# Kernel tuning notes

Hardware: AMD Instinct MI355X
Metric: run time of the kernel (lower is better)

The kernel has to match this reference:

```python
import jax, jax.numpy as jnp
import numpy as np

D = 768          # model dim (ViT-Base)
H = 12           # num heads
DH = 64          # head dim
DFF = 4 * D      # mlp hidden
SMAX = 1024      # max sequence length in the packed batch
LENS = np.array([1024, 896, 768, 640, 512, 448, 256, 64], dtype=np.int32)
TOTAL = int(LENS.sum())  # 4608
LN_EPS = 1e-6
NEG = -1e30


def _ln(x, w, b):
    mu = jnp.mean(x, axis=-1, keepdims=True)
    var = jnp.mean(jnp.square(x - mu), axis=-1, keepdims=True)
    return (x - mu) * jax.lax.rsqrt(var + LN_EPS) * w + b


def setup_inputs() -> dict:
    key = jax.random.key(0)
    ks = jax.random.split(key, 16)
    s = 0.02
    cu = jnp.asarray(np.concatenate([[0], np.cumsum(LENS)]).astype(np.int32))
    return {
        "x": jax.random.normal(ks[0], (TOTAL, D), jnp.float32),
        "norm1_w": jnp.ones((D,), jnp.float32),
        "norm1_b": jnp.zeros((D,), jnp.float32),
        "qkv_w": jax.random.normal(ks[1], (3 * D, D), jnp.float32) * s,
        "qkv_b": jnp.zeros((3 * D,), jnp.float32),
        "proj_w": jax.random.normal(ks[2], (D, D), jnp.float32) * s,
        "proj_b": jnp.zeros((D,), jnp.float32),
        "ls1_gamma": jax.random.normal(ks[3], (D,), jnp.float32) * 0.1,
        "norm2_w": jnp.ones((D,), jnp.float32),
        "norm2_b": jnp.zeros((D,), jnp.float32),
        "fc1_w": jax.random.normal(ks[4], (DFF, D), jnp.float32) * s,
        "fc1_b": jnp.zeros((DFF,), jnp.float32),
        "fc2_w": jax.random.normal(ks[5], (D, DFF), jnp.float32) * s,
        "fc2_b": jnp.zeros((D,), jnp.float32),
        "ls2_gamma": jax.random.normal(ks[6], (D,), jnp.float32) * 0.1,
        "cu_seqlens": cu,
    }


def reference(x, norm1_w, norm1_b, qkv_w, qkv_b, proj_w, proj_b, ls1_gamma,
              norm2_w, norm2_b, fc1_w, fc1_b, fc2_w, fc2_b, ls2_gamma,
              cu_seqlens):
    total = x.shape[0]
    B = cu_seqlens.shape[0] - 1
    tok = jnp.arange(total)
    seg = jnp.searchsorted(cu_seqlens[1:], tok, side="right")  # [Total]
    pos = tok - cu_seqlens[seg]                                 # [Total]
    lens = cu_seqlens[1:] - cu_seqlens[:-1]                     # [B]

    # --- attention branch ---
    xn = _ln(x, norm1_w, norm1_b)
    qkv = (xn @ qkv_w.T + qkv_b).reshape(total, 3, H, DH)
    q, k, v = qkv[:, 0], qkv[:, 1], qkv[:, 2]                   # [Total,H,DH]

    # pad packed ragged tokens to [B, SMAX, H, DH]
    def pad(t):
        return jnp.zeros((B, SMAX, H, DH), t.dtype).at[seg, pos].set(t)
    qp, kp, vp = pad(q), pad(k), pad(v)

    valid = jnp.arange(SMAX)[None, :] < lens[:, None]           # [B,SMAX]
    scores = jnp.einsum("bqhd,bkhd->bhqk", qp, kp) * (DH ** -0.5)
    scores = jnp.where(valid[:, None, None, :], scores, NEG)
    attn = jax.nn.softmax(scores, axis=-1)
    out = jnp.einsum("bhqk,bkhd->bqhd", attn, vp)
    out = out[seg, pos].reshape(total, D)                       # back to packed

    attn_out = out @ proj_w.T + proj_b
    x = x + ls1_gamma * attn_out

    # --- mlp branch ---
    xn2 = _ln(x, norm2_w, norm2_b)
    h = jax.nn.gelu(xn2 @ fc1_w.T + fc1_b, approximate=False)
    h = h @ fc2_w.T + fc2_b
    return x + ls2_gamma * h
```

## Files before the change

### kernel.cpp

```cpp
#include <hip/hip_runtime.h>
#include <hip/hip_bf16.h>
#include <stdint.h>

#define D 768
#define HEADS 12
#define DHEAD 64
#define DFF 3072
#define TOTAL 4608
#define NSEG 8

typedef __bf16 bf16;
typedef __bf16 bf16x8 __attribute__((ext_vector_type(8)));
typedef __bf16 bf16x4 __attribute__((ext_vector_type(4)));
typedef float f32x4 __attribute__((ext_vector_type(4)));

__device__ __forceinline__ void gld_lds16(const void* g, void* l) {
  __builtin_amdgcn_global_load_lds(
      (const __attribute__((address_space(1))) void*)g,
      (__attribute__((address_space(3))) void*)(uintptr_t)l, 16, 0, 0);
}

__global__ __launch_bounds__(256) void cvt_all_kernel(
    const float* __restrict__ a, const float* __restrict__ b,
    const float* __restrict__ c, const float* __restrict__ d,
    bf16* __restrict__ out, int nA, int nAB, int nABC, int nTot) {
  int i = blockIdx.x * blockDim.x + threadIdx.x;
  if (i >= nTot) return;
  const float* src;
  int j;
  if (i < nA) { src = a; j = i; }
  else if (i < nAB) { src = b; j = i - nA; }
  else if (i < nABC) { src = c; j = i - nAB; }
  else { src = d; j = i - nABC; }
  float4 v = ((const float4*)src)[j];
  bf16x4 o;
  o[0] = (bf16)v.x; o[1] = (bf16)v.y; o[2] = (bf16)v.z; o[3] = (bf16)v.w;
  ((bf16x4*)out)[i] = o;
}

__global__ __launch_bounds__(256) void ln_kernel(
    const float* __restrict__ x, const float* __restrict__ w,
    const float* __restrict__ b, bf16* __restrict__ out) {
  __shared__ float red[8];
  int row = blockIdx.x;
  const float* xr = x + (size_t)row * D;
  int t = threadIdx.x;
  float v[3];
  float s = 0.f, s2 = 0.f;
#pragma unroll
  for (int j = 0; j < 3; j++) {
    v[j] = xr[t + 256 * j];
    s += v[j]; s2 += v[j] * v[j];
  }
#pragma unroll
  for (int m = 1; m <= 32; m <<= 1) {
    s += __shfl_xor(s, m);
    s2 += __shfl_xor(s2, m);
  }
  int wave = t >> 6, lane = t & 63;
  if (lane == 0) { red[wave] = s; red[4 + wave] = s2; }
  __syncthreads();
  s = red[0] + red[1] + red[2] + red[3];
  s2 = red[4] + red[5] + red[6] + red[7];
  float mu = s * (1.f / 768.f);
  float var = s2 * (1.f / 768.f) - mu * mu;
  float rstd = rsqrtf(var + 1e-6f);
#pragma unroll
  for (int j = 0; j < 3; j++) {
    int c = t + 256 * j;
    out[(size_t)row * D + c] = (bf16)((v[j] - mu) * rstd * w[c] + b[c]);
  }
}

__device__ __forceinline__ float fast_gelu(float v) {
  float u = v * (0.7978845608f + 0.0356774081f * v * v);
  float e = exp2f(2.8853900818f * u);
  float th = 1.f - 2.f * __builtin_amdgcn_rcpf(1.f + e);
  return 0.5f * v * (1.f + th);
}

template <int MODE, int TN, int BK, int GX, int GY>
__global__ __launch_bounds__(512, 4) void gemm_kernel(
    const bf16* __restrict__ A, const bf16* __restrict__ W,
    const float* __restrict__ bias, const float* __restrict__ res,
    const float* __restrict__ gamma, bf16* __restrict__ outb,
    float* __restrict__ outf, int N, int K) {
  constexpr int WNW = (TN == 128) ? 4 : 2;
  constexpr int WMW = 8 / WNW;
  constexpr int MI = 128 / 16 / WMW;
  constexpr int NJ = TN / 16 / WNW;
  constexpr int KH = BK / 32;
  constexpr int CG = BK / 8;
  constexpr int SH = 0;
  constexpr int LPR = BK / 8;
  constexpr int RS = 64 / LPR;
  constexpr int RA = 128 / 8;
  constexpr int RB = TN / 8;
  __shared__ __align__(16) bf16 As[2][128 * BK];
  __shared__ __align__(16) bf16 Bs[2][TN * BK];

  const int g = blockIdx.x;
  const int xc = g & 7, q = g >> 3;
  const int bx = q % GX, by = xc + 8 * (q / GX);
  if (by >= GY) return;
  const int m0 = by * 128, n0 = bx * TN;

  const int t = threadIdx.x, wave = t >> 6, lane = t & 63;
  const int quad = lane >> 4, l16 = lane & 15;
  const int wm = (wave % WMW) * (MI * 16), wn = (wave / WMW) * (NJ * 16);

  const int ar = lane / LPR, ac = lane % LPR;
  const int acg = ac ^ (((wave * RA + ar) >> SH) & (CG - 1));
  const int bcg = ac ^ (((wave * RB + ar) >> SH) & (CG - 1));
  const bf16* gA = A + (size_t)(m0 + wave * RA + ar) * K + acg * 8;
  const bf16* gB = W + (size_t)(n0 + wave * RB + ar) * K + bcg * 8;

  auto stage = [&](int buf) {
#pragma unroll
    for (int n = 0; n < RA / RS; n++)
      gld_lds16(gA + (size_t)n * RS * K, &As[buf][(wave * RA + n * RS) * BK]);
#pragma unroll
    for (int n = 0; n < RB / RS; n++)
      gld_lds16(gB + (size_t)n * RS * K, &Bs[buf][(wave * RB + n * RS) * BK]);
    gA += BK; gB += BK;
  };

  stage(0);

  f32x4 acc[MI][NJ] = {};
  int cur = 0;
  for (int k0 = 0; k0 < K; k0 += BK) {
    __syncthreads();
    if (k0 + BK < K) stage(cur ^ 1);
    const bf16* as = As[cur];
    const bf16* bs = Bs[cur];
    bf16x8 af[KH][MI], bg[KH][NJ];
#pragma unroll
    for (int kh = 0; kh < KH; kh++) {
#pragma unroll
      for (int i = 0; i < MI; i++) {
        int R = wm + i * 16 + l16;
        af[kh][i] = *(const bf16x8*)&as[R * BK + 8 * ((kh * 4 + quad) ^ ((R >> SH) & (CG - 1)))];
      }
#pragma unroll
      for (int j = 0; j < NJ; j++) {
        int R = wn + j * 16 + l16;
        bg[kh][j] = *(const bf16x8*)&bs[R * BK + 8 * ((kh * 4 + quad) ^ ((R >> SH) & (CG - 1)))];
      }
    }
#pragma unroll
    for (int kh = 0; kh < KH; kh++)
#pragma unroll
      for (int i = 0; i < MI; i++)
#pragma unroll
        for (int j = 0; j < NJ; j++)
          acc[i][j] = __builtin_amdgcn_mfma_f32_16x16x32_bf16(af[kh][i], bg[kh][j], acc[i][j], 0, 0, 0);
    cur ^= 1;
  }

#pragma unroll
  for (int i = 0; i < MI; i++)
#pragma unroll
    for (int j = 0; j < NJ; j++)
#pragma unroll
      for (int r = 0; r < 4; r++) {
        int row = m0 + wm + i * 16 + quad * 4 + r;
        int col = n0 + wn + j * 16 + l16;
        float v = acc[i][j][r] + bias[col];
        if (MODE == 0) {
          outb[(size_t)row * N + col] = (bf16)v;
        } else if (MODE == 1) {
          outf[(size_t)row * N + col] = res[(size_t)row * N + col] + gamma[col] * v;
        } else {
          outb[(size_t)row * N + col] = (bf16)fast_gelu(v);
        }
      }
}

#define KCH 8
#define QT2 52

__global__ __launch_bounds__(256) void attn_kernel(
    const bf16* __restrict__ qkv, const int* __restrict__ cu,
    bf16* __restrict__ attn, float* __restrict__ Opart,
    float* __restrict__ lpart) {
  __shared__ __align__(16) bf16 Ks[64][72];
  __shared__ __align__(16) bf16 VTs[64][64];

  const int qt = blockIdx.x, h = blockIdx.y, ch = blockIdx.z;
  const int tok0 = qt * 64;
  int b = 0;
  while (cu[b + 1] <= tok0) b++;
  const int s0 = cu[b], S = cu[b + 1] - s0;

  const int ntile = S >> 6;
  const int nchunk = (ntile + KCH - 1) / KCH;
  if (ch >= nchunk) return;
  const int t0 = ch * KCH;
  const int t1 = (t0 + KCH < ntile) ? t0 + KCH : ntile;

  const int t = threadIdx.x, wave = t >> 6, lane = t & 63;
  const int quad = lane >> 4, l16 = lane & 15;

  const size_t qrow = (size_t)(tok0 + wave * 16 + l16) * (3 * D) + h * 64;
  const bf16x8 bq0 = *(const bf16x8*)&qkv[qrow + quad * 8];
  const bf16x8 bq1 = *(const bf16x8*)&qkv[qrow + 32 + quad * 8];

  const int srow = t >> 2, sc0 = (t & 3) * 16;
  const size_t kbase = (size_t)(s0 + srow) * (3 * D) + h * 64 + sc0 + D;
  const int vr0 = (t & 15) * 4, vd0 = (t >> 4) * 4;
  const size_t vbase = (size_t)(s0 + vr0) * (3 * D) + h * 64 + vd0 + 2 * D;
  const int kB0 = ((vr0 >> 5) << 5) | (((vr0 >> 2) & 3) << 3) | (((vr0 >> 4) & 1) << 2);

  bf16x8 kr0 = *(const bf16x8*)&qkv[kbase + (size_t)t0 * 64 * (3 * D)];
  bf16x8 kr1 = *(const bf16x8*)&qkv[kbase + (size_t)t0 * 64 * (3 * D) + 8];
  bf16x4 vp[4];
#pragma unroll
  for (int i = 0; i < 4; i++)
    vp[i] = *(const bf16x4*)&qkv[vbase + (size_t)t0 * 64 * (3 * D) + (size_t)i * (3 * D)];

  f32x4 Oacc[4] = {};
  float li = 0.f;
  const float SC = 0.125f * 1.44269504089f;
  const int vsw = (l16 & 7) * 8;

  for (int it = t0; it < t1; it++) {
    __syncthreads();
    *(bf16x8*)&Ks[srow][sc0] = kr0;
    *(bf16x8*)&Ks[srow][sc0 + 8] = kr1;
#pragma unroll
    for (int j = 0; j < 4; j++) {
      int d = vd0 + j;
      bf16x4 w;
      w[0] = vp[0][j]; w[1] = vp[1][j]; w[2] = vp[2][j]; w[3] = vp[3][j];
      *(bf16x4*)&VTs[d][kB0 ^ ((d & 7) * 8)] = w;
    }
    __syncthreads();

    if (it + 1 < t1) {
      const size_t koff = kbase + (size_t)(it + 1) * 64 * (3 * D);
      const size_t voff = vbase + (size_t)(it + 1) * 64 * (3 * D);
      kr0 = *(const bf16x8*)&qkv[koff];
      kr1 = *(const bf16x8*)&qkv[koff + 8];
#pragma unroll
      for (int i = 0; i < 4; i++)
        vp[i] = *(const bf16x4*)&qkv[voff + (size_t)i * (3 * D)];
    }

    f32x4 sac[4];
#pragma unroll
    for (int nt = 0; nt < 4; nt++) {
      bf16x8 ak0 = *(const bf16x8*)&Ks[nt * 16 + l16][quad * 8];
      bf16x8 ak1 = *(const bf16x8*)&Ks[nt * 16 + l16][32 + quad * 8];
      f32x4 z = {};
      z = __builtin_amdgcn_mfma_f32_16x16x32_bf16(ak0, bq0, z, 0, 0, 0);
      sac[nt] = __builtin_amdgcn_mfma_f32_16x16x32_bf16(ak1, bq1, z, 0, 0, 0);
    }

    bf16x8 bv0, bv1;
    float ls = 0.f;
#pragma unroll
    for (int r = 0; r < 4; r++) {
      float e0 = exp2f(sac[0][r] * SC);
      float e1 = exp2f(sac[1][r] * SC);
      float e2 = exp2f(sac[2][r] * SC);
      float e3 = exp2f(sac[3][r] * SC);
      ls += (e0 + e1) + (e2 + e3);
      bv0[r] = (bf16)e0; bv0[4 + r] = (bf16)e1;
      bv1[r] = (bf16)e2; bv1[4 + r] = (bf16)e3;
    }
    li += ls;

#pragma unroll
    for (int dt = 0; dt < 4; dt++) {
      bf16x8 av0 = *(const bf16x8*)&VTs[dt * 16 + l16][(quad * 8) ^ vsw];
      bf16x8 av1 = *(const bf16x8*)&VTs[dt * 16 + l16][(32 + quad * 8) ^ vsw];
      Oacc[dt] = __builtin_amdgcn_mfma_f32_16x16x32_bf16(av0, bv0, Oacc[dt], 0, 0, 0);
      Oacc[dt] = __builtin_amdgcn_mfma_f32_16x16x32_bf16(av1, bv1, Oacc[dt], 0, 0, 0);
    }
  }

  li += __shfl_xor(li, 16);
  li += __shfl_xor(li, 32);
  const int q = wave * 16 + l16;

  if (nchunk == 1) {
    const float inv = 1.f / li;
#pragma unroll
    for (int dt = 0; dt < 4; dt++) {
      bf16x4 w;
#pragma unroll
      for (int r = 0; r < 4; r++) w[r] = (bf16)(Oacc[dt][r] * inv);
      *(bf16x4*)&attn[(size_t)(tok0 + q) * D + h * 64 + dt * 16 + quad * 4] = w;
    }
  } else {
    const int slot = (h * QT2 + qt) * 2 + ch;
    float* op = Opart + (size_t)slot * 4096;
#pragma unroll
    for (int dt = 0; dt < 4; dt++)
      *(f32x4*)&op[q * 64 + dt * 16 + quad * 4] = Oacc[dt];
    if (quad == 0) lpart[(size_t)slot * 64 + q] = li;
  }
}

__global__ __launch_bounds__(256) void attn_reduce_kernel(
    const float* __restrict__ Opart, const float* __restrict__ lpart,
    const int* __restrict__ cu, bf16* __restrict__ attn) {
  const int qt = blockIdx.x, h = blockIdx.y;
  const int tok0 = qt * 64;
  int b = 0;
  while (cu[b + 1] <= tok0) b++;
  const int ntile = (cu[b + 1] - cu[b]) >> 6;
  if (ntile <= KCH) return;

  const int t = threadIdx.x, q = t >> 2, c0 = (t & 3) * 16;
  const int slot0 = (h * QT2 + qt) * 2;
  const float li = lpart[(size_t)slot0 * 64 + q] + lpart[(size_t)(slot0 + 1) * 64 + q];
  const float inv = 1.f / li;
  const float* p0 = Opart + (size_t)slot0 * 4096 + q * 64 + c0;
  const float* p1 = p0 + 4096;
  bf16x8 o0, o1;
#pragma unroll
  for (int g = 0; g < 4; g++) {
    f32x4 a = *(const f32x4*)&p0[g * 4];
    f32x4 c = *(const f32x4*)&p1[g * 4];
#pragma unroll
    for (int r = 0; r < 4; r++) {
      bf16 v = (bf16)((a[r] + c[r]) * inv);
      if (g < 2) o0[g * 4 + r] = v; else o1[(g - 2) * 4 + r] = v;
    }
  }
  const size_t ob = (size_t)(tok0 + q) * D + h * 64 + c0;
  *(bf16x8*)&attn[ob] = o0;
  *(bf16x8*)&attn[ob + 8] = o1;
}

extern "C" void kernel_launch(void* const* d_in, const int* in_sizes, int n_in,
                              void* d_out, int out_size, void* d_ws,
                              size_t ws_size, hipStream_t stream) {
  const float* x       = (const float*)d_in[0];
  const float* norm1_w = (const float*)d_in[1];
  const float* norm1_b = (const float*)d_in[2];
  const float* qkv_w   = (const float*)d_in[3];
  const float* qkv_b   = (const float*)d_in[4];
  const float* proj_w  = (const float*)d_in[5];
  const float* proj_b  = (const float*)d_in[6];
  const float* ls1     = (const float*)d_in[7];
  const float* norm2_w = (const float*)d_in[8];
  const float* norm2_b = (const float*)d_in[9];
  const float* fc1_w   = (const float*)d_in[10];
  const float* fc1_b   = (const float*)d_in[11];
  const float* fc2_w   = (const float*)d_in[12];
  const float* fc2_b   = (const float*)d_in[13];
  const float* ls2     = (const float*)d_in[14];
  const int*   cu      = (const int*)d_in[15];
  float* out = (float*)d_out;

  char* ws = (char*)d_ws;
  size_t off = 0;
  auto alloc = [&](size_t bytes) {
    void* p = ws + off;
    off += (bytes + 255) & ~(size_t)255;
    return p;
  };
  bf16* w_qkv  = (bf16*)alloc((size_t)3 * D * D * 2);
  bf16* w_proj = (bf16*)alloc((size_t)D * D * 2);
  bf16* w_fc1  = (bf16*)alloc((size_t)DFF * D * 2);
  bf16* w_fc2  = (bf16*)alloc((size_t)D * DFF * 2);
  bf16* xn     = (bf16*)alloc((size_t)TOTAL * D * 2);
  bf16* qkv    = (bf16*)alloc((size_t)TOTAL * 3 * D * 2);
  bf16* attnb  = (bf16*)alloc((size_t)TOTAL * D * 2);
  float* x1    = (float*)alloc((size_t)TOTAL * D * 4);
  float* Opart = (float*)alloc((size_t)QT2 * HEADS * 2 * 4096 * 4);
  float* lpart = (float*)alloc((size_t)QT2 * HEADS * 2 * 64 * 4);
  bf16* hbuf   = qkv;

  {
    int nA   = 3 * D * D / 4;
    int nAB  = nA + D * D / 4;
    int nABC = nAB + DFF * D / 4;
    int nTot = nABC + D * DFF / 4;
    cvt_all_kernel<<<(nTot + 255) / 256, 256, 0, stream>>>(
        qkv_w, proj_w, fc1_w, fc2_w, w_qkv, nA, nAB, nABC, nTot);
  }

  ln_kernel<<<TOTAL, 256, 0, stream>>>(x, norm1_w, norm1_b, xn);

  constexpr int GY = TOTAL / 128;
  constexpr int GYP = ((GY + 7) / 8) * 8;

  gemm_kernel<0, 128, 64, 18, GY><<<18 * GYP, 512, 0, stream>>>(
      xn, w_qkv, qkv_b, nullptr, nullptr, qkv, nullptr, 3 * D, D);

  dim3 ga(TOTAL / 64, HEADS, 2);
  attn_kernel<<<ga, 256, 0, stream>>>(qkv, cu, attnb, Opart, lpart);
  attn_reduce_kernel<<<dim3(QT2, HEADS), 256, 0, stream>>>(Opart, lpart, cu, attnb);

  gemm_kernel<1, 64, 64, 12, GY><<<12 * GYP, 512, 0, stream>>>(
      attnb, w_proj, proj_b, x, ls1, nullptr, x1, D, D);

  ln_kernel<<<TOTAL, 256, 0, stream>>>(x1, norm2_w, norm2_b, xn);

  gemm_kernel<2, 128, 64, 24, GY><<<24 * GYP, 512, 0, stream>>>(
      xn, w_fc1, fc1_b, nullptr, nullptr, hbuf, nullptr, DFF, D);

  gemm_kernel<1, 64, 64, 12, GY><<<12 * GYP, 512, 0, stream>>>(
      hbuf, w_fc2, fc2_b, x1, ls2, nullptr, out, D, DFF);
}
```

Before: 261.0 us.

## Triple-buffer GEMM pipeline, use 64-wide tiles everywhere, fuse LN1 with weight cast

The GEMM moves from a double-buffered LDS ring to a triple-buffered one. It waits with explicit vmcnt counts so two stages of global-to-LDS loads stay in flight while the current tile is computed. The kernel is now specialised to TN=BK=64, so the QKV and FC1 GEMMs switch from 128-wide to 64-wide N tiles, which doubles their grid. The first LayerNorm and the weight fp32-to-bf16 conversion are merged into one launch to save a kernel launch and let the two overlap. The cost is more LDS per block and smaller per-block tiles for the wide GEMMs, which lowers operand reuse.

After: 271.7 us. 1.04x slower.

```diff
diff --git a/kernel.cpp b/kernel.cpp
--- a/kernel.cpp
+++ b/kernel.cpp
@@ -20,22 +20,56 @@
       (__attribute__((address_space(3))) void*)(uintptr_t)l, 16, 0, 0);
 }
 
-__global__ __launch_bounds__(256) void cvt_all_kernel(
-    const float* __restrict__ a, const float* __restrict__ b,
-    const float* __restrict__ c, const float* __restrict__ d,
-    bf16* __restrict__ out, int nA, int nAB, int nABC, int nTot) {
-  int i = blockIdx.x * blockDim.x + threadIdx.x;
-  if (i >= nTot) return;
-  const float* src;
-  int j;
-  if (i < nA) { src = a; j = i; }
-  else if (i < nAB) { src = b; j = i - nA; }
-  else if (i < nABC) { src = c; j = i - nAB; }
-  else { src = d; j = i - nABC; }
-  float4 v = ((const float4*)src)[j];
-  bf16x4 o;
-  o[0] = (bf16)v.x; o[1] = (bf16)v.y; o[2] = (bf16)v.z; o[3] = (bf16)v.w;
-  ((bf16x4*)out)[i] = o;
+__global__ __launch_bounds__(256) void prep_kernel(
+    const float* __restrict__ x, const float* __restrict__ w,
+    const float* __restrict__ b, bf16* __restrict__ xn,
+    const float* __restrict__ wa, const float* __restrict__ wb,
+    const float* __restrict__ wc, const float* __restrict__ wd,
+    bf16* __restrict__ wout, int nA, int nAB, int nABC, int nTot) {
+  __shared__ float red[8];
+  const int t = threadIdx.x;
+  if (blockIdx.x >= TOTAL) {
+    int i = (blockIdx.x - TOTAL) * 256 + t;
+    if (i >= nTot) return;
+    const float* src;
+    int j;
+    if (i < nA) { src = wa; j = i; }
+    else if (i < nAB) { src = wb; j = i - nA; }
+    else if (i < nABC) { src = wc; j = i - nAB; }
+    else { src = wd; j = i - nABC; }
+    float4 v = ((const float4*)src)[j];
+    bf16x4 o;
+    o[0] = (bf16)v.x; o[1] = (bf16)v.y; o[2] = (bf16)v.z; o[3] = (bf16)v.w;
+    ((bf16x4*)wout)[i] = o;
+    return;
+  }
+  const int row = blockIdx.x;
+  const float* xr = x + (size_t)row * D;
+  float v[3];
+  float s = 0.f, s2 = 0.f;
+#pragma unroll
+  for (int j = 0; j < 3; j++) {
+    v[j] = xr[t + 256 * j];
+    s += v[j]; s2 += v[j] * v[j];
+  }
+#pragma unroll
+  for (int m = 1; m <= 32; m <<= 1) {
+    s += __shfl_xor(s, m);
+    s2 += __shfl_xor(s2, m);
+  }
+  int wave = t >> 6, lane = t & 63;
+  if (lane == 0) { red[wave] = s; red[4 + wave] = s2; }
+  __syncthreads();
+  s = red[0] + red[1] + red[2] + red[3];
+  s2 = red[4] + red[5] + red[6] + red[7];
+  float mu = s * (1.f / 768.f);
+  float var = s2 * (1.f / 768.f) - mu * mu;
+  float rstd = rsqrtf(var + 1e-6f);
+#pragma unroll
+  for (int j = 0; j < 3; j++) {
+    int c = t + 256 * j;
+    xn[(size_t)row * D + c] = (bf16)((v[j] - mu) * rstd * w[c] + b[c]);
+  }
 }
 
 __global__ __launch_bounds__(256) void ln_kernel(
@@ -85,19 +119,15 @@
     const float* __restrict__ bias, const float* __restrict__ res,
     const float* __restrict__ gamma, bf16* __restrict__ outb,
     float* __restrict__ outf, int N, int K) {
-  constexpr int WNW = (TN == 128) ? 4 : 2;
-  constexpr int WMW = 8 / WNW;
-  constexpr int MI = 128 / 16 / WMW;
-  constexpr int NJ = TN / 16 / WNW;
+  static_assert(TN == 64 && BK == 64, "pipeline tuned for TN=BK=64");
+  constexpr int MI = 2;
+  constexpr int NJ = 2;
   constexpr int KH = BK / 32;
   constexpr int CG = BK / 8;
-  constexpr int SH = 0;
-  constexpr int LPR = BK / 8;
-  constexpr int RS = 64 / LPR;
-  constexpr int RA = 128 / 8;
-  constexpr int RB = TN / 8;
-  __shared__ __align__(16) bf16 As[2][128 * BK];
-  __shared__ __align__(16) bf16 Bs[2][TN * BK];
+  constexpr int RA = 16;
+  constexpr int RB = 8;
+  __shared__ __align__(16) bf16 As[3][128 * BK];
+  __shared__ __align__(16) bf16 Bs[3][TN * BK];
 
   const int g = blockIdx.x;
   const int xc = g & 7, q = g >> 3;
@@ -107,45 +137,51 @@
 
   const int t = threadIdx.x, wave = t >> 6, lane = t & 63;
   const int quad = lane >> 4, l16 = lane & 15;
-  const int wm = (wave % WMW) * (MI * 16), wn = (wave / WMW) * (NJ * 16);
-
-  const int ar = lane / LPR, ac = lane % LPR;
-  const int acg = ac ^ (((wave * RA + ar) >> SH) & (CG - 1));
-  const int bcg = ac ^ (((wave * RB + ar) >> SH) & (CG - 1));
+  const int wm = (wave & 3) * 32, wn = (wave >> 2) * 32;
+
+  const int ar = lane >> 3, ac = lane & 7;
+  const int acg = ac ^ ((wave * RA + ar) & (CG - 1));
+  const int bcg = ac ^ ((wave * RB + ar) & (CG - 1));
   const bf16* gA = A + (size_t)(m0 + wave * RA + ar) * K + acg * 8;
   const bf16* gB = W + (size_t)(n0 + wave * RB + ar) * K + bcg * 8;
 
   auto stage = [&](int buf) {
-#pragma unroll
-    for (int n = 0; n < RA / RS; n++)
-      gld_lds16(gA + (size_t)n * RS * K, &As[buf][(wave * RA + n * RS) * BK]);
-#pragma unroll
-    for (int n = 0; n < RB / RS; n++)
-      gld_lds16(gB + (size_t)n * RS * K, &Bs[buf][(wave * RB + n * RS) * BK]);
+    gld_lds16(gA, &As[buf][(wave * RA) * BK]);
+    gld_lds16(gA + (size_t)8 * K, &As[buf][(wave * RA + 8) * BK]);
+    gld_lds16(gB, &Bs[buf][(wave * RB) * BK]);
     gA += BK; gB += BK;
   };
 
   stage(0);
-
+  stage(1);
+
+  const int NIT = K / BK;
   f32x4 acc[MI][NJ] = {};
-  int cur = 0;
-  for (int k0 = 0; k0 < K; k0 += BK) {
-    __syncthreads();
-    if (k0 + BK < K) stage(cur ^ 1);
-    const bf16* as = As[cur];
-    const bf16* bs = Bs[cur];
+  int c = 0;
+  for (int it = 0; it < NIT; it++) {
+    if (it + 1 < NIT)
+      asm volatile("s_waitcnt vmcnt(3)" ::: "memory");
+    else
+      asm volatile("s_waitcnt vmcnt(0)" ::: "memory");
+    __builtin_amdgcn_s_barrier();
+    if (it + 2 < NIT) {
+      int nb = c + 2; if (nb >= 3) nb -= 3;
+      stage(nb);
+    }
+    const bf16* as = As[c];
+    const bf16* bs = Bs[c];
     bf16x8 af[KH][MI], bg[KH][NJ];
 #pragma unroll
     for (int kh = 0; kh < KH; kh++) {
 #pragma unroll
       for (int i = 0; i < MI; i++) {
         int R = wm + i * 16 + l16;
-        af[kh][i] = *(const bf16x8*)&as[R * BK + 8 * ((kh * 4 + quad) ^ ((R >> SH) & (CG - 1)))];
+        af[kh][i] = *(const bf16x8*)&as[R * BK + 8 * ((kh * 4 + quad) ^ (R & (CG - 1)))];
       }
 #pragma unroll
       for (int j = 0; j < NJ; j++) {
         int R = wn + j * 16 + l16;
-        bg[kh][j] = *(const bf16x8*)&bs[R * BK + 8 * ((kh * 4 + quad) ^ ((R >> SH) & (CG - 1)))];
+        bg[kh][j] = *(const bf16x8*)&bs[R * BK + 8 * ((kh * 4 + quad) ^ (R & (CG - 1)))];
       }
     }
 #pragma unroll
@@ -155,7 +191,7 @@
 #pragma unroll
         for (int j = 0; j < NJ; j++)
           acc[i][j] = __builtin_amdgcn_mfma_f32_16x16x32_bf16(af[kh][i], bg[kh][j], acc[i][j], 0, 0, 0);
-    cur ^= 1;
+    c = (c == 2) ? 0 : c + 1;
   }
 
 #pragma unroll
@@ -380,16 +416,15 @@
     int nAB  = nA + D * D / 4;
     int nABC = nAB + DFF * D / 4;
     int nTot = nABC + D * DFF / 4;
-    cvt_all_kernel<<<(nTot + 255) / 256, 256, 0, stream>>>(
-        qkv_w, proj_w, fc1_w, fc2_w, w_qkv, nA, nAB, nABC, nTot);
-  }
-
-  ln_kernel<<<TOTAL, 256, 0, stream>>>(x, norm1_w, norm1_b, xn);
+    prep_kernel<<<TOTAL + (nTot + 255) / 256, 256, 0, stream>>>(
+        x, norm1_w, norm1_b, xn, qkv_w, proj_w, fc1_w, fc2_w, w_qkv,
+        nA, nAB, nABC, nTot);
+  }
 
   constexpr int GY = TOTAL / 128;
   constexpr int GYP = ((GY + 7) / 8) * 8;
 
-  gemm_kernel<0, 128, 64, 18, GY><<<18 * GYP, 512, 0, stream>>>(
+  gemm_kernel<0, 64, 64, 36, GY><<<36 * GYP, 512, 0, stream>>>(
       xn, w_qkv, qkv_b, nullptr, nullptr, qkv, nullptr, 3 * D, D);
 
   dim3 ga(TOTAL / 64, HEADS, 2);
@@ -401,7 +436,7 @@
 
   ln_kernel<<<TOTAL, 256, 0, stream>>>(x1, norm2_w, norm2_b, xn);
 
-  gemm_kernel<2, 128, 64, 24, GY><<<24 * GYP, 512, 0, stream>>>(
+  gemm_kernel<2, 64, 64, 48, GY><<<48 * GYP, 512, 0, stream>>>(
       xn, w_fc1, fc1_b, nullptr, nullptr, hbuf, nullptr, DFF, D);
 
   gemm_kernel<1, 64, 64, 12, GY><<<12 * GYP, 512, 0, stream>>>(
```
